# Kernel optimization log

Measured on AMD Instinct MI355X. Metric: run time of the kernel, lower is better.

The kernel has to match this reference:

```python
import jax, jax.numpy as jnp
import numpy as np

# ---- dimensions ----
N = 16384      # nodes
E = 131072     # edges (avg degree 8)
F = 128        # scalar channel width == s_dim
L = 9          # spherical-harmonic components (lmax=2)
R = 8          # radial basis size
DOUT = L * F   # post-product node width (1152)
K = 1024       # fixed number of master nodes (static stand-in for m>0.5)
HID = 64       # master-selection hidden dim
DA = 64        # virtual-attention head dim
LAMBDA_ATTN = 0.5
R_CUT = 5.0
EPS = 1e-9


def sh_l2(u):
    # real SH polynomials up to l=2 on unit vectors u[..., 3] -> [..., 9]
    x, y, z = u[..., 0], u[..., 1], u[..., 2]
    o = jnp.ones_like(x)
    return jnp.stack([o, x, y, z, x * y, y * z, 3.0 * z * z - 1.0, x * z, x * x - y * y], axis=-1)


def bessel(r):
    # Bessel radial basis; r [..., 1] -> [..., R]
    n = jnp.arange(1, R + 1, dtype=r.dtype)
    return jnp.sqrt(2.0 / R_CUT) * jnp.sin(n * jnp.pi * r / R_CUT) / jnp.maximum(r, EPS)


def setup_inputs() -> dict:
    key = jax.random.key(0)
    ks = jax.random.split(key, 18)
    s = lambda d: 1.0 / np.sqrt(d)
    return {
        'h': jax.random.normal(ks[0], (N, F), jnp.float32),
        'pos': 3.0 * jax.random.normal(ks[1], (N, 3), jnp.float32),
        'edge_sh': jax.random.normal(ks[2], (E, L), jnp.float32),
        'edge_feats': jax.random.uniform(ks[3], (E, R), jnp.float32),
        'W_node_l': s(F) * jax.random.normal(ks[4], (F, F), jnp.float32),
        'W_rad_l': s(R) * jax.random.normal(ks[5], (R, F), jnp.float32),
        'W_prod_l': s(L * F) * jax.random.normal(ks[6], (L, F, DOUT), jnp.float32),
        'ms_W1': s(F) * jax.random.normal(ks[7], (F, HID), jnp.float32),
        'ms_b1': jnp.zeros((HID,), jnp.float32),
        'ms_W2': s(HID) * jax.random.normal(ks[8], (HID, 1), jnp.float32),
        'ms_b2': jnp.zeros((1,), jnp.float32),
        'vg_Wq': s(F) * jax.random.normal(ks[9], (F, DA), jnp.float32),
        'vg_Wk': s(F) * jax.random.normal(ks[10], (F, DA), jnp.float32),
        'W_node_h': s(DOUT) * jax.random.normal(ks[11], (DOUT, F), jnp.float32),
        'W_rad_h': s(R) * jax.random.normal(ks[12], (R, F), jnp.float32),
        'W_prod_h': s(L * F) * jax.random.normal(ks[13], (L, F, DOUT), jnp.float32),
        'edge_index': jax.random.randint(ks[14], (2, E), 0, N),
    }


def reference(h, pos, edge_sh, edge_feats, W_node_l, W_rad_l, W_prod_l,
              ms_W1, ms_b1, ms_W2, ms_b2, vg_Wq, vg_Wk,
              W_node_h, W_rad_h, W_prod_h, edge_index):
    src, dst = edge_index[0], edge_index[1]

    # ---- local conv + reshape + prod (with padded residual sc) ----
    t = (h[src] @ W_node_l) * (edge_feats @ W_rad_l)                      # [E,F]
    msg = edge_sh[:, :, None] * t[:, None, :]                             # [E,L,F]
    upd = jax.ops.segment_sum(msg, dst, num_segments=N)                   # [N,L,F]
    sc = jnp.pad(h, ((0, 0), (0, DOUT - F)))
    h_local = jnp.einsum('nlf,lfg->ng', upd, W_prod_l) + sc               # [N,DOUT]

    # ---- master selection (MLP -> sigmoid); fixed top-K masters ----
    hs = h_local[:, :F]
    m = jax.nn.sigmoid(jax.nn.relu(hs @ ms_W1 + ms_b1) @ ms_W2 + ms_b2)[:, 0]  # [N]
    _, midx = jax.lax.top_k(m, K)
    master_idx = jnp.sort(midx)                                           # [K]

    # ---- induced subgraph among masters as dense [K,K] adjacency ----
    rank = jnp.full((N,), K, dtype=jnp.int32).at[master_idx].set(jnp.arange(K, dtype=jnp.int32))
    adj = jnp.zeros((K + 1, K + 1), h.dtype).at[rank[src], rank[dst]].max(jnp.ones((E,), h.dtype))
    adj_induced = adj[:K, :K]

    h_m = h_local[master_idx]                                             # [K,DOUT]
    pos_m = pos[master_idx]                                               # [K,3]
    hms = h_m[:, :F]

    # ---- virtual graph generation (attention -> thresholded dense adj) ----
    q = hms @ vg_Wq
    kk = hms @ vg_Wk
    A = jax.nn.sigmoid(q @ kk.T / jnp.sqrt(jnp.asarray(DA, h.dtype)))     # [K,K]
    A_virtual = jnp.where(A > LAMBDA_ATTN, A, 0.0)
    eye = jnp.eye(K, dtype=bool)
    Bv = (A_virtual > 0) & ~eye                                           # remove self loops
    Bv = Bv | Bv.T                                                        # to_undirected
    adj_master = jnp.clip(adj_induced + Bv.astype(h.dtype), 0.0, 1.0) * (1.0 - jnp.eye(K, dtype=h.dtype))

    # ---- hierarchical conv over dense master graph ----
    A_rec = adj_master.T                                                  # A_rec[i,j]=1: sender j -> receiver i
    V = pos_m[None, :, :] - pos_m[:, None, :]                             # vec = pos[src]-pos[dst]
    r = jnp.linalg.norm(V, axis=-1, keepdims=True)                        # [K,K,1]
    u = V / jnp.maximum(r, EPS)
    sh_m = sh_l2(u)                                                       # [K,K,L]
    rad = bessel(r)                                                       # [K,K,R]
    tm = (h_m @ W_node_h)[None, :, :] * (rad @ W_rad_h) * A_rec[:, :, None]  # [K,K,F]
    upd_m = jnp.einsum('ijl,ijf->ilf', sh_m, tm)                          # [K,L,F]
    h_hier = jnp.einsum('ilf,lfg->ig', upd_m, W_prod_h) + h_m             # sc_master pad is 0-width

    # ---- masked scatter blend ----
    h_exp = jnp.zeros_like(h_local).at[master_idx].set(h_hier)
    h_final = (1.0 - m[:, None]) * h_local + m[:, None] * h_exp
    return (h_final, A_virtual, m, master_idx)
```

## Files before the change

### kernel.cpp

```cpp
#include <hip/hip_runtime.h>
#include <hip/hip_bf16.h>
#include <stdint.h>

#define N_NODES 16384
#define E_EDGES 131072
#define F_DIM 128
#define L_DIM 9
#define R_DIM 8
#define DOUT_DIM 1152
#define K_SEL 1024
#define HID_DIM 64
#define DA_DIM 64

typedef unsigned short u16;
typedef __attribute__((ext_vector_type(8))) short bf16x8;
typedef __attribute__((ext_vector_type(4))) float f32x4;

static __device__ inline u16 f2bs(float x) {
  union { __hip_bfloat16 b; u16 s; } u;
  u.b = __float2bfloat16(x);
  return u.s;
}

#define GLDS16(gsrc, ldst) __builtin_amdgcn_global_load_lds( \
    (__attribute__((address_space(1))) void*)(void*)(gsrc),  \
    (__attribute__((address_space(3))) void*)(ldst), 16, 0, 0)

__global__ __launch_bounds__(256) void gemm_mfma(
    const float* __restrict__ A, const u16* __restrict__ Bt,
    float* __restrict__ C, int ldc, int M, int Nc, int Kc,
    const float* __restrict__ Add, int ldadd, int addW)
{
  __shared__ float Af[128 * 32];
  __shared__ u16  Bs[128 * 32];
  const int tid = threadIdx.x;
  const int wave = tid >> 6, lane = tid & 63;
  const int wm = wave >> 1, wn = wave & 1;
  const int l15 = lane & 15, quad = lane >> 4;
  const int bm = blockIdx.y * 128, bn = blockIdx.x * 128;

  f32x4 acc[4][4];
#pragma unroll
  for (int i = 0; i < 4; i++)
#pragma unroll
    for (int j = 0; j < 4; j++) acc[i][j] = (f32x4)(0.f);

  for (int k0 = 0; k0 < Kc; k0 += 32) {
    __syncthreads();
#pragma unroll
    for (int it = 0; it < 4; it++) {
      int c = it * 256 + tid;
      int row = c >> 3, op = c & 7;
      int oct = op ^ (row & 7);
      const float* g = A + (size_t)(bm + row) * Kc + k0 + oct * 4;
      GLDS16(g, &Af[c * 4]);
    }
#pragma unroll
    for (int it = 0; it < 2; it++) {
      int c = it * 256 + tid;
      int row = c >> 2, qp = c & 3;
      int q = qp ^ ((row >> 1) & 3);
      const u16* g = Bt + (size_t)(bn + row) * Kc + k0 + q * 8;
      GLDS16(g, &Bs[c * 8]);
    }
    __syncthreads();

    bf16x8 af[4], bfg[4];
#pragma unroll
    for (int mi = 0; mi < 4; mi++) {
      int m = wm * 64 + mi * 16 + l15;
      int o0 = (quad * 2) ^ (m & 7), o1 = (quad * 2 + 1) ^ (m & 7);
      float4 lo = *(const float4*)&Af[m * 32 + o0 * 4];
      float4 hi = *(const float4*)&Af[m * 32 + o1 * 4];
      bf16x8 r;
      r[0] = (short)f2bs(lo.x); r[1] = (short)f2bs(lo.y);
      r[2] = (short)f2bs(lo.z); r[3] = (short)f2bs(lo.w);
      r[4] = (short)f2bs(hi.x); r[5] = (short)f2bs(hi.y);
      r[6] = (short)f2bs(hi.z); r[7] = (short)f2bs(hi.w);
      af[mi] = r;
    }
#pragma unroll
    for (int ni = 0; ni < 4; ni++) {
      int n = wn * 64 + ni * 16 + l15;
      int q2 = quad ^ ((n >> 1) & 3);
      bfg[ni] = *(const bf16x8*)&Bs[n * 32 + q2 * 8];
    }
#pragma unroll
    for (int mi = 0; mi < 4; mi++)
#pragma unroll
      for (int ni = 0; ni < 4; ni++)
        acc[mi][ni] = __builtin_amdgcn_mfma_f32_16x16x32_bf16(af[mi], bfg[ni], acc[mi][ni], 0, 0, 0);
  }
#pragma unroll
  for (int mi = 0; mi < 4; mi++)
#pragma unroll
    for (int ni = 0; ni < 4; ni++)
#pragma unroll
      for (int r = 0; r < 4; r++) {
        int row = bm + wm * 64 + mi * 16 + quad * 4 + r;
        int col = bn + wn * 64 + ni * 16 + l15;
        float v = acc[mi][ni][r];
        if (Add != nullptr && col < addW) v += Add[(size_t)row * ldadd + col];
        C[(size_t)row * ldc + col] = v;
      }
}

__global__ __launch_bounds__(256) void gemm_mfma_b16(
    const u16* __restrict__ A, const u16* __restrict__ Bt,
    float* __restrict__ C, int ldc, int Kc, int nbx, int nwg,
    const float* __restrict__ Add, int ldadd, int addW)
{
  __shared__ u16 As[2][128 * 32];
  __shared__ u16 Bs[2][128 * 32];
  const int tid = threadIdx.x;
  const int wave = tid >> 6, lane = tid & 63;
  const int wm = wave >> 1, wn = wave & 1;
  const int l15 = lane & 15, quad = lane >> 4;
  const int lin = blockIdx.x;
  const int swz = (lin & 7) * (nwg >> 3) + (lin >> 3);
  const int bm = (swz / nbx) * 128, bn = (swz % nbx) * 128;

  const int c0 = tid,      r0 = c0 >> 2, q0 = (c0 & 3) ^ ((r0 >> 1) & 3);
  const int c1 = 256 + tid, r1 = c1 >> 2, q1 = (c1 & 3) ^ ((r1 >> 1) & 3);
  const u16* gA0 = A + (size_t)(bm + r0) * Kc + q0 * 8;
  const u16* gA1 = A + (size_t)(bm + r1) * Kc + q1 * 8;
  const u16* gB0 = Bt + (size_t)(bn + r0) * Kc + q0 * 8;
  const u16* gB1 = Bt + (size_t)(bn + r1) * Kc + q1 * 8;

  f32x4 acc[4][4];
#pragma unroll
  for (int i = 0; i < 4; i++)
#pragma unroll
    for (int j = 0; j < 4; j++) acc[i][j] = (f32x4)(0.f);

#define STAGE_AB(s, k0) do {                      \
    GLDS16(gA0 + (k0), &As[s][c0 * 8]);           \
    GLDS16(gA1 + (k0), &As[s][c1 * 8]);           \
    GLDS16(gB0 + (k0), &Bs[s][c0 * 8]);           \
    GLDS16(gB1 + (k0), &Bs[s][c1 * 8]);           \
  } while (0)

  STAGE_AB(0, 0);
  __syncthreads();
  int cur = 0;
  const int nt = Kc / 32;
  for (int t = 0; t < nt; t++) {
    if (t + 1 < nt) STAGE_AB(cur ^ 1, (t + 1) * 32);
    bf16x8 af[4], bfg[4];
#pragma unroll
    for (int mi = 0; mi < 4; mi++) {
      int m = wm * 64 + mi * 16 + l15;
      af[mi] = *(const bf16x8*)&As[cur][m * 32 + (quad ^ ((m >> 1) & 3)) * 8];
    }
#pragma unroll
    for (int ni = 0; ni < 4; ni++) {
      int n = wn * 64 + ni * 16 + l15;
      bfg[ni] = *(const bf16x8*)&Bs[cur][n * 32 + (quad ^ ((n >> 1) & 3)) * 8];
    }
#pragma unroll
    for (int mi = 0; mi < 4; mi++)
#pragma unroll
      for (int ni = 0; ni < 4; ni++)
        acc[mi][ni] = __builtin_amdgcn_mfma_f32_16x16x32_bf16(af[mi], bfg[ni], acc[mi][ni], 0, 0, 0);
    __syncthreads();
    cur ^= 1;
  }
#undef STAGE_AB

#pragma unroll
  for (int mi = 0; mi < 4; mi++)
#pragma unroll
    for (int ni = 0; ni < 4; ni++)
#pragma unroll
      for (int r = 0; r < 4; r++) {
        int row = bm + wm * 64 + mi * 16 + quad * 4 + r;
        int col = bn + wn * 64 + ni * 16 + l15;
        float v = acc[mi][ni][r];
        if (Add != nullptr && col < addW) v += Add[(size_t)row * ldadd + col];
        C[(size_t)row * ldc + col] = v;
      }
}

__global__ __launch_bounds__(256) void transpose_bf16(
    const float* __restrict__ W, u16* __restrict__ Bt, int K, int N)
{
  __shared__ float t[32][33];
  const int n0 = blockIdx.x * 32, k0 = blockIdx.y * 32;
  const int tx = threadIdx.x & 31, ty = threadIdx.x >> 5;
  for (int r = ty; r < 32; r += 8) t[r][tx] = W[(size_t)(k0 + r) * N + n0 + tx];
  __syncthreads();
  for (int r = ty; r < 32; r += 8) Bt[(size_t)(n0 + r) * K + k0 + tx] = f2bs(t[tx][r]);
}

__global__ __launch_bounds__(256) void hs_gemm_kernel(
    const float* __restrict__ A,
    const float* __restrict__ B,
    float* __restrict__ psum)
{
  __shared__ float As[16][129];
  __shared__ float Bs[16][128];
  const int tid = threadIdx.x;
  const int tx = tid & 15, ty = tid >> 4;
  const int bm = blockIdx.x * 128;
  const int z = blockIdx.y;
  const int kb = z * (DOUT_DIM / 4);
  const int ke = kb + DOUT_DIM / 4;
  const int ac = tid & 15, ar0 = tid >> 4;
  const int bc = tid & 127, br0 = tid >> 7;
  float acc[8][8];
#pragma unroll
  for (int i = 0; i < 8; i++)
#pragma unroll
    for (int j = 0; j < 8; j++) acc[i][j] = 0.f;

  float ra[8], rb[8];
#define LOADREG(k0) do {                                                       \
    _Pragma("unroll")                                                          \
    for (int rr = 0; rr < 8; rr++)                                             \
      ra[rr] = A[(size_t)(bm + ar0 + rr * 16) * DOUT_DIM + (k0) + ac];         \
    _Pragma("unroll")                                                          \
    for (int rr = 0; rr < 8; rr++)                                             \
      rb[rr] = B[(size_t)((k0) + br0 + rr * 2) * DOUT_DIM + bc];               \
  } while (0)

  LOADREG(kb);
  for (int k0 = kb; k0 < ke; k0 += 16) {
#pragma unroll
    for (int rr = 0; rr < 8; rr++) As[ac][ar0 + rr * 16] = ra[rr];
#pragma unroll
    for (int rr = 0; rr < 8; rr++) Bs[br0 + rr * 2][bc] = rb[rr];
    __syncthreads();
    if (k0 + 16 < ke) LOADREG(k0 + 16);
#pragma unroll
    for (int kk = 0; kk < 16; kk++) {
      float a[8], b[8];
#pragma unroll
      for (int i = 0; i < 8; i++) a[i] = As[kk][ty * 8 + i];
#pragma unroll
      for (int j = 0; j < 8; j++) b[j] = Bs[kk][tx * 8 + j];
#pragma unroll
      for (int i = 0; i < 8; i++)
#pragma unroll
        for (int j = 0; j < 8; j++) acc[i][j] = fmaf(a[i], b[j], acc[i][j]);
    }
    __syncthreads();
  }
#undef LOADREG
#pragma unroll
  for (int i = 0; i < 8; i++) {
    size_t row = (size_t)z * N_NODES + bm + ty * 8 + i;
#pragma unroll
    for (int j = 0; j < 8; j++)
      psum[row * F_DIM + tx * 8 + j] = acc[i][j];
  }
}

__global__ __launch_bounds__(256) void hs_reduce_kernel(
    const float* __restrict__ psum, const float* __restrict__ h, float* __restrict__ hs)
{
  size_t i4 = (size_t)blockIdx.x * 256 + threadIdx.x;
  const size_t stride = (size_t)N_NODES * F_DIM / 4;
  const float4* p = (const float4*)psum;
  float4 a = p[i4], b = p[i4 + stride], c = p[i4 + 2 * stride], d = p[i4 + 3 * stride];
  float4 hh = ((const float4*)h)[i4];
  float4 o;
  o.x = a.x + b.x + c.x + d.x + hh.x;
  o.y = a.y + b.y + c.y + d.y + hh.y;
  o.z = a.z + b.z + c.z + d.z + hh.z;
  o.w = a.w + b.w + c.w + d.w + hh.w;
  ((float4*)hs)[i4] = o;
}

__global__ __launch_bounds__(256) void gemm64_f32(
    const float* __restrict__ A, int lda,
    const float* __restrict__ B, int ldb,
    float* __restrict__ C, int ldc,
    int M, int Nc, int Kc, int kPerSplit,
    const float* __restrict__ Add, int ldadd, int addW)
{
  __shared__ float As[16][65];
  __shared__ float Bs[16][64];
  const int tid = threadIdx.x;
  const int tx = tid & 15, ty = tid >> 4;
  const int bm = blockIdx.y * 64, bn = blockIdx.x * 64;
  const int kb = blockIdx.z * kPerSplit;
  const int ke = min(kb + kPerSplit, Kc);
  float acc[4][4];
#pragma unroll
  for (int i = 0; i < 4; i++)
#pragma unroll
    for (int j = 0; j < 4; j++) acc[i][j] = 0.f;
  for (int k0 = kb; k0 < ke; k0 += 16) {
    const int ac = tid & 15, ar = tid >> 4;
#pragma unroll
    for (int rr = 0; rr < 4; rr++) {
      int row = ar + rr * 16;
      As[ac][row] = A[(size_t)(bm + row) * lda + k0 + ac];
    }
    const int bc = tid & 63, br = tid >> 6;
#pragma unroll
    for (int rr = 0; rr < 4; rr++) {
      int kr = br + rr * 4;
      Bs[kr][bc] = B[(size_t)(k0 + kr) * ldb + bn + bc];
    }
    __syncthreads();
#pragma unroll
    for (int kk = 0; kk < 16; kk++) {
      float a[4], b[4];
#pragma unroll
      for (int i = 0; i < 4; i++) a[i] = As[kk][ty * 4 + i];
#pragma unroll
      for (int j = 0; j < 4; j++) b[j] = Bs[kk][tx * 4 + j];
#pragma unroll
      for (int i = 0; i < 4; i++)
#pragma unroll
        for (int j = 0; j < 4; j++) acc[i][j] = fmaf(a[i], b[j], acc[i][j]);
    }
    __syncthreads();
  }
#pragma unroll
  for (int i = 0; i < 4; i++) {
    int row = bm + ty * 4 + i;
#pragma unroll
    for (int j = 0; j < 4; j++) {
      int col = bn + tx * 4 + j;
      if (gridDim.z > 1) {
        atomicAdd(&C[(size_t)row * ldc + col], acc[i][j]);
      } else {
        float v = acc[i][j];
        if (Add != nullptr && col < addW) v += Add[(size_t)row * ldadd + col];
        C[(size_t)row * ldc + col] = v;
      }
    }
  }
}

__global__ __launch_bounds__(256) void count_kernel(
    const int* __restrict__ ei, int* __restrict__ counts)
{
  int e = blockIdx.x * 256 + threadIdx.x;
  atomicAdd(&counts[ei[E_EDGES + e]], 1);
}

__global__ __launch_bounds__(1024) void scan_kernel(
    const int* __restrict__ counts, int* __restrict__ offsets, int* __restrict__ cursor)
{
  __shared__ int part[1024];
  const int t = threadIdx.x;
  const int base = t * 16;
  int loc[16];
  int s = 0;
#pragma unroll
  for (int k = 0; k < 16; k++) { loc[k] = counts[base + k]; s += loc[k]; }
  part[t] = s;
  __syncthreads();
  for (int d = 1; d < 1024; d <<= 1) {
    int v = (t >= d) ? part[t - d] : 0;
    __syncthreads();
    part[t] += v;
    __syncthreads();
  }
  int run = part[t] - s;
#pragma unroll
  for (int k = 0; k < 16; k++) {
    offsets[base + k] = run;
    cursor[base + k] = run;
    run += loc[k];
  }
}

__global__ __launch_bounds__(256) void fill_kernel(
    const int* __restrict__ ei, int* __restrict__ cursor, int* __restrict__ elist)
{
  int e = blockIdx.x * 256 + threadIdx.x;
  int d = ei[E_EDGES + e];
  int p = atomicAdd(&cursor[d], 1);
  elist[p] = e;
}

__global__ __launch_bounds__(128) void gather_accum_kernel(
    const float* __restrict__ hW, const float* __restrict__ edge_sh,
    const float* __restrict__ edge_feats, const float* __restrict__ W_rad_l,
    const int* __restrict__ ei, const int* __restrict__ offsets,
    const int* __restrict__ counts, const int* __restrict__ elist,
    float* __restrict__ upd, u16* __restrict__ updb)
{
  const int d = blockIdx.x, f = threadIdx.x;
  const float w0 = W_rad_l[0 * F_DIM + f], w1 = W_rad_l[1 * F_DIM + f];
  const float w2 = W_rad_l[2 * F_DIM + f], w3 = W_rad_l[3 * F_DIM + f];
  const float w4 = W_rad_l[4 * F_DIM + f], w5 = W_rad_l[5 * F_DIM + f];
  const float w6 = W_rad_l[6 * F_DIM + f], w7 = W_rad_l[7 * F_DIM + f];
  const int b = offsets[d], n = counts[d];
  float acc[L_DIM];
#pragma unroll
  for (int l = 0; l < L_DIM; l++) acc[l] = 0.f;
  for (int k = 0; k < n; k++) {
    const int e = elist[b + k];
    const int s = ei[e];
    const float4 ef0 = *(const float4*)&edge_feats[(size_t)e * R_DIM];
    const float4 ef1 = *(const float4*)&edge_feats[(size_t)e * R_DIM + 4];
    float rw = ef0.x * w0;
    rw = fmaf(ef0.y, w1, rw); rw = fmaf(ef0.z, w2, rw); rw = fmaf(ef0.w, w3, rw);
    rw = fmaf(ef1.x, w4, rw); rw = fmaf(ef1.y, w5, rw);
    rw = fmaf(ef1.z, w6, rw); rw = fmaf(ef1.w, w7, rw);
    const float tf = hW[(size_t)s * F_DIM + f] * rw;
#pragma unroll
    for (int l = 0; l < L_DIM; l++)
      acc[l] = fmaf(edge_sh[(size_t)e * L_DIM + l], tf, acc[l]);
  }
#pragma unroll
  for (int l = 0; l < L_DIM; l++)
    upd[(size_t)d * DOUT_DIM + l * F_DIM + f] = acc[l];
  if (updb != nullptr) {
#pragma unroll
    for (int l = 0; l < L_DIM; l++)
      updb[(size_t)d * DOUT_DIM + l * F_DIM + f] = f2bs(acc[l]);
  }
}

__global__ __launch_bounds__(256) void gate_kernel(
    const float* __restrict__ hs, const float* __restrict__ W1,
    const float* __restrict__ b1, const float* __restrict__ W2,
    const float* __restrict__ b2, float* __restrict__ m_ws, float* __restrict__ m_out,
    int* __restrict__ hist1)
{
  __shared__ float sW1[F_DIM * HID_DIM];
  __shared__ float srow[4][F_DIM];
  const int tid = threadIdx.x;
  for (int t = tid; t < F_DIM * HID_DIM; t += 256) sW1[t] = W1[t];
  const int wave = tid >> 6, lane = tid & 63;
  const int n = blockIdx.x * 4 + wave;
  srow[wave][lane] = hs[(size_t)n * F_DIM + lane];
  srow[wave][lane + 64] = hs[(size_t)n * F_DIM + lane + 64];
  __syncthreads();
  float hid = b1[lane];
#pragma unroll 8
  for (int c = 0; c < F_DIM; c++) hid = fmaf(srow[wave][c], sW1[c * HID_DIM + lane], hid);
  hid = fmaxf(hid, 0.f);
  float v = hid * W2[lane];
#pragma unroll
  for (int off = 32; off > 0; off >>= 1) v += __shfl_down(v, off);
  if (lane == 0) {
    float mm = 1.f / (1.f + expf(-(v + b2[0])));
    m_ws[n] = mm;
    m_out[n] = mm;
    unsigned mb = __float_as_uint(mm);
    atomicAdd(&hist1[mb >> 16], 1);
  }
}

__global__ __launch_bounds__(1024) void radix_sel_kernel(
    const int* __restrict__ hist, const int* __restrict__ kin, int kinIdx,
    int* __restrict__ outp, int outIdx)
{
  __shared__ int part[1024];
  const int t = threadIdx.x;
  const int Kv = kin ? kin[kinIdx] : K_SEL;
  const int base = t * 64;
  int s = 0;
  for (int k = 0; k < 64; k++) s += hist[base + k];
  part[t] = s;
  __syncthreads();
  for (int d = 1; d < 1024; d <<= 1) {
    int v = (t + d < 1024) ? part[t + d] : 0;
    __syncthreads();
    part[t] += v;
    __syncthreads();
  }
  int inc = part[t];
  if (inc >= Kv && inc - s < Kv) {
    int r = inc - s;
    for (int b = base + 63; b >= base; b--) {
      int hv = hist[b];
      if (r + hv >= Kv) { outp[outIdx] = b; outp[outIdx + 1] = Kv - r; break; }
      r += hv;
    }
  }
}

__global__ __launch_bounds__(256) void hist2_kernel(
    const float* __restrict__ m_ws, const int* __restrict__ selb, int* __restrict__ hist2)
{
  int i = blockIdx.x * 256 + threadIdx.x;
  unsigned mb = __float_as_uint(m_ws[i]);
  if ((int)(mb >> 16) == selb[0]) atomicAdd(&hist2[mb & 0xFFFFu], 1);
}

__global__ __launch_bounds__(256) void flag_kernel(
    const float* __restrict__ m_ws, int* __restrict__ selb,
    unsigned char* __restrict__ flags, int* __restrict__ cand)
{
  int i = blockIdx.x * 256 + threadIdx.x;
  unsigned mb = __float_as_uint(m_ws[i]);
  unsigned vb = ((unsigned)selb[0] << 16) | (unsigned)selb[2];
  unsigned char fl = 0;
  if (mb > vb) fl = 1;
  else if (mb == vb) { int p = atomicAdd(&selb[4], 1); cand[p] = i; }
  flags[i] = fl;
}

__global__ __launch_bounds__(1024) void cand_kernel(
    const int* __restrict__ selb, const int* __restrict__ cand, unsigned char* __restrict__ flags)
{
  const int nc = selb[4], need = selb[3];
  for (int c = threadIdx.x; c < nc; c += 1024) {
    const int idx = cand[c];
    int r = 0;
    for (int o = 0; o < nc; o++) r += (cand[o] < idx) ? 1 : 0;
    if (r < need) flags[idx] = 1;
  }
}

__global__ __launch_bounds__(1024) void compact_kernel(
    const unsigned char* __restrict__ flags, int* __restrict__ midx,
    int* __restrict__ rank, float* __restrict__ mi_out)
{
  __shared__ int part[1024];
  const int t = threadIdx.x;
  const int base = t * 16;
  int loc[16];
  int s = 0;
#pragma unroll
  for (int k = 0; k < 16; k++) { loc[k] = flags[base + k]; s += loc[k]; }
  part[t] = s;
  __syncthreads();
  for (int d = 1; d < 1024; d <<= 1) {
    int v = (t >= d) ? part[t - d] : 0;
    __syncthreads();
    part[t] += v;
    __syncthreads();
  }
  int run = part[t] - s;
#pragma unroll
  for (int k = 0; k < 16; k++) {
    int i = base + k;
    if (loc[k]) {
      midx[run] = i;
      mi_out[run] = (float)i;
      rank[i] = run;
      run++;
    } else {
      rank[i] = K_SEL;
    }
  }
}

__global__ __launch_bounds__(256) void adj_kernel(
    const int* __restrict__ ei, const int* __restrict__ rank, unsigned char* __restrict__ adjm)
{
  int e = blockIdx.x * 256 + threadIdx.x;
  int rs = rank[ei[e]];
  int rd = rank[ei[E_EDGES + e]];
  if (rs < K_SEL && rd < K_SEL) adjm[(size_t)rs * K_SEL + rd] = 1;
}

__global__ __launch_bounds__(128) void gather_kernel(
    const float* __restrict__ hl, const float* __restrict__ pos,
    const int* __restrict__ midx, float* __restrict__ h_m, float* __restrict__ pos_m)
{
  const int rI = blockIdx.x, t = threadIdx.x;
  const int mi = midx[rI];
  const float4* src = (const float4*)(hl + (size_t)mi * DOUT_DIM);
  float4* dst = (float4*)(h_m + (size_t)rI * DOUT_DIM);
  for (int c = t; c < DOUT_DIM / 4; c += 128) dst[c] = src[c];
  if (t < 3) pos_m[rI * 3 + t] = pos[mi * 3 + t];
}

__global__ __launch_bounds__(128) void qk_kernel(
    const float* __restrict__ hs, const int* __restrict__ midx,
    const float* __restrict__ Wq, const float* __restrict__ Wk,
    float* __restrict__ q, float* __restrict__ kk)
{
  __shared__ float row[F_DIM];
  const int i = blockIdx.x, t = threadIdx.x;
  const int mi = midx[i];
  row[t] = hs[(size_t)mi * F_DIM + t];
  __syncthreads();
  const int d = t & 63;
  const float* W = (t < 64) ? Wq : Wk;
  float acc = 0.f;
#pragma unroll 8
  for (int c = 0; c < F_DIM; c++) acc = fmaf(row[c], W[c * DA_DIM + d], acc);
  float* dst = (t < 64) ? q : kk;
  dst[(size_t)i * DA_DIM + d] = acc;
}

__global__ __launch_bounds__(256) void attn_kernel(
    const float* __restrict__ q, const float* __restrict__ kk,
    unsigned char* __restrict__ maskA, float* __restrict__ Av)
{
  __shared__ float qs[16][DA_DIM + 1], ks[16][DA_DIM + 1];
  const int tx = threadIdx.x, ty = threadIdx.y;
  const int tid = ty * 16 + tx;
  const int i0 = blockIdx.y * 16, j0 = blockIdx.x * 16;
  for (int t = tid; t < 16 * DA_DIM; t += 256) {
    int rr = t >> 6, cc = t & 63;
    qs[rr][cc] = q[(size_t)(i0 + rr) * DA_DIM + cc];
    ks[rr][cc] = kk[(size_t)(j0 + rr) * DA_DIM + cc];
  }
  __syncthreads();
  float acc = 0.f;
#pragma unroll
  for (int d2 = 0; d2 < DA_DIM; d2++) acc = fmaf(qs[ty][d2], ks[tx][d2], acc);
  float sgl = 1.f / (1.f + expf(-acc * 0.125f));
  size_t o = (size_t)(i0 + ty) * K_SEL + (j0 + tx);
  bool big = sgl > 0.5f;
  maskA[o] = big ? 1 : 0;
  Av[o] = big ? sgl : 0.f;
}

__global__ __launch_bounds__(256) void listbuild_kernel(
    const unsigned char* __restrict__ adjm, const unsigned char* __restrict__ maskA,
    u16* __restrict__ list, int* __restrict__ nj)
{
  __shared__ int cnt;
  const int i = blockIdx.x, tid = threadIdx.x;
  const int lane = tid & 63;
  if (tid == 0) cnt = 0;
  __syncthreads();
#pragma unroll
  for (int jt = 0; jt < 4; jt++) {
    int j = jt * 256 + tid;
    bool e = (j != i) && (adjm[(size_t)j * K_SEL + i] | maskA[(size_t)j * K_SEL + i] |
                          maskA[(size_t)i * K_SEL + j]);
    unsigned long long m = __ballot(e);
    int nset = __popcll(m);
    int base = 0;
    if (lane == 0 && nset) base = atomicAdd(&cnt, nset);
    base = __shfl(base, 0);
    if (e) {
      int p = base + __popcll(m & ((1ull << lane) - 1ull));
      list[(size_t)i * K_SEL + p] = (u16)j;
    }
  }
  __syncthreads();
  if (tid == 0) nj[i] = cnt;
}

__global__ __launch_bounds__(512) void hier2_kernel(
    const float* __restrict__ hWn, const float* __restrict__ pos_m,
    const float* __restrict__ W_rad_h, const u16* __restrict__ list,
    const int* __restrict__ nj, float* __restrict__ upd_m, u16* __restrict__ updb_m)
{
  __shared__ float gsm[128][20];
  __shared__ float red[3][L_DIM][F_DIM];
  const int tid = threadIdx.x;
  const int i = blockIdx.x;
  const int f = tid & 127, jsub = tid >> 7;
  const float sw0 = W_rad_h[0 * F_DIM + f], sw1 = W_rad_h[1 * F_DIM + f];
  const float sw2 = W_rad_h[2 * F_DIM + f], sw3 = W_rad_h[3 * F_DIM + f];
  const float sw4 = W_rad_h[4 * F_DIM + f], sw5 = W_rad_h[5 * F_DIM + f];
  const float sw6 = W_rad_h[6 * F_DIM + f], sw7 = W_rad_h[7 * F_DIM + f];
  const float pix = pos_m[i * 3 + 0], piy = pos_m[i * 3 + 1], piz = pos_m[i * 3 + 2];
  float acc[L_DIM];
#pragma unroll
  for (int l = 0; l < L_DIM; l++) acc[l] = 0.f;
  const int n = nj[i];
  for (int c0 = 0; c0 < n; c0 += 128) {
    const int cnt = min(128, n - c0);
    __syncthreads();
    if (tid < cnt) {
      const int j = list[(size_t)i * K_SEL + c0 + tid];
      float vx = pos_m[j * 3 + 0] - pix;
      float vy = pos_m[j * 3 + 1] - piy;
      float vz = pos_m[j * 3 + 2] - piz;
      float r = sqrtf(vx * vx + vy * vy + vz * vz);
      float rm = fmaxf(r, 1e-9f);
      float inv = 1.f / rm;
      float ux = vx * inv, uy = vy * inv, uz = vz * inv;
      float theta = 0.62831853071795864769f * r;
      float s1 = sinf(theta), c1 = cosf(theta);
      float coef = 0.632455532033675866f * inv;
      float snm2 = 0.f, snm1 = s1;
      gsm[tid][0] = s1 * coef;
#pragma unroll
      for (int nn = 2; nn <= R_DIM; nn++) {
        float sn = 2.f * c1 * snm1 - snm2;
        gsm[tid][nn - 1] = sn * coef;
        snm2 = snm1; snm1 = sn;
      }
      gsm[tid][8] = 1.f; gsm[tid][9] = ux; gsm[tid][10] = uy; gsm[tid][11] = uz;
      gsm[tid][12] = ux * uy; gsm[tid][13] = uy * uz;
      gsm[tid][14] = 3.f * uz * uz - 1.f;
      gsm[tid][15] = ux * uz; gsm[tid][16] = ux * ux - uy * uy;
      gsm[tid][17] = __int_as_float(j);
      gsm[tid][18] = 0.f; gsm[tid][19] = 0.f;
    }
    __syncthreads();
    for (int t = jsub; t < cnt; t += 4) {
      float2 s2 = *(const float2*)&gsm[t][16];
      const int j = __float_as_int(s2.y);
      const float hw = hWn[(size_t)j * F_DIM + f];
      float4 r0 = *(const float4*)&gsm[t][0];
      float4 r1 = *(const float4*)&gsm[t][4];
      float4 s0 = *(const float4*)&gsm[t][8];
      float4 s1g = *(const float4*)&gsm[t][12];
      float rw = r0.x * sw0;
      rw = fmaf(r0.y, sw1, rw); rw = fmaf(r0.z, sw2, rw); rw = fmaf(r0.w, sw3, rw);
      rw = fmaf(r1.x, sw4, rw); rw = fmaf(r1.y, sw5, rw);
      rw = fmaf(r1.z, sw6, rw); rw = fmaf(r1.w, sw7, rw);
      const float tm = hw * rw;
      acc[0] = fmaf(s0.x, tm, acc[0]); acc[1] = fmaf(s0.y, tm, acc[1]);
      acc[2] = fmaf(s0.z, tm, acc[2]); acc[3] = fmaf(s0.w, tm, acc[3]);
      acc[4] = fmaf(s1g.x, tm, acc[4]); acc[5] = fmaf(s1g.y, tm, acc[5]);
      acc[6] = fmaf(s1g.z, tm, acc[6]); acc[7] = fmaf(s1g.w, tm, acc[7]);
      acc[8] = fmaf(s2.x, tm, acc[8]);
    }
  }
  __syncthreads();
  if (jsub > 0) {
#pragma unroll
    for (int l = 0; l < L_DIM; l++) red[jsub - 1][l][f] = acc[l];
  }
  __syncthreads();
  if (jsub == 0) {
#pragma unroll
    for (int l = 0; l < L_DIM; l++) {
      float v = acc[l] + red[0][l][f] + red[1][l][f] + red[2][l][f];
      upd_m[(size_t)i * DOUT_DIM + l * F_DIM + f] = v;
      updb_m[(size_t)i * DOUT_DIM + l * F_DIM + f] = f2bs(v);
    }
  }
}

__global__ __launch_bounds__(256) void combine_kernel(
    float* __restrict__ out0, const float* __restrict__ h_hier,
    const float* __restrict__ m_ws, const int* __restrict__ rank)
{
  size_t i4 = (size_t)blockIdx.x * 256 + threadIdx.x;
  int n = (int)(i4 / (DOUT_DIM / 4));
  int g4 = (int)(i4 % (DOUT_DIM / 4));
  float mv = m_ws[n];
  int r = rank[n];
  float4 hl = ((const float4*)out0)[i4];
  float4 he = make_float4(0.f, 0.f, 0.f, 0.f);
  if (r < K_SEL) he = ((const float4*)h_hier)[(size_t)r * (DOUT_DIM / 4) + g4];
  float4 o;
  o.x = (1.f - mv) * hl.x + mv * he.x;
  o.y = (1.f - mv) * hl.y + mv * he.y;
  o.z = (1.f - mv) * hl.z + mv * he.z;
  o.w = (1.f - mv) * hl.w + mv * he.w;
  ((float4*)out0)[i4] = o;
}

extern "C" void kernel_launch(void* const* d_in, const int* in_sizes, int n_in,
                              void* d_out, int out_size, void* d_ws, size_t ws_size,
                              hipStream_t stream)
{
  const float* h         = (const float*)d_in[0];
  const float* pos       = (const float*)d_in[1];
  const float* edge_sh   = (const float*)d_in[2];
  const float* edge_feats= (const float*)d_in[3];
  const float* W_node_l  = (const float*)d_in[4];
  const float* W_rad_l   = (const float*)d_in[5];
  const float* W_prod_l  = (const float*)d_in[6];
  const float* ms_W1     = (const float*)d_in[7];
  const float* ms_b1     = (const float*)d_in[8];
  const float* ms_W2     = (const float*)d_in[9];
  const float* ms_b2     = (const float*)d_in[10];
  const float* vg_Wq     = (const float*)d_in[11];
  const float* vg_Wk     = (const float*)d_in[12];
  const float* W_node_h  = (const float*)d_in[13];
  const float* W_rad_h   = (const float*)d_in[14];
  const float* W_prod_h  = (const float*)d_in[15];
  const int*   eidx      = (const int*)d_in[16];

  float* out    = (float*)d_out;
  float* out_hf = out;
  float* out_Av = out + (size_t)N_NODES * DOUT_DIM;
  float* out_m  = out_Av + (size_t)K_SEL * K_SEL;
  float* out_mi = out_m + N_NODES;

  char* ws = (char*)d_ws;
  float* upd = (float*)ws;
  float* hW  = (float*)(ws + (size_t)N_NODES * DOUT_DIM * 4);
  float* hs  = hW;
  const size_t updbOff = (size_t)N_NODES * DOUT_DIM * 4 + (size_t)N_NODES * F_DIM * 4;
  const size_t updbNeed = updbOff + (size_t)N_NODES * DOUT_DIM * 2;
  const bool useB16 = (ws_size >= updbNeed);
  u16* updb = (u16*)(ws + updbOff);
  float* psum = out_hf;
  u16* Btl = (u16*)out_Av;
  char* csr = (char*)out_Av + (((size_t)DOUT_DIM * DOUT_DIM * 2 + 255) & ~(size_t)255);
  int* counts  = (int*)csr;
  int* offsets = counts + N_NODES;
  int* cursor  = offsets + N_NODES;
  int* elist   = cursor + N_NODES;
  size_t off = 0;
  auto alloc = [&](size_t bytes) -> void* {
    void* p = ws + off;
    off += (bytes + 255) & ~(size_t)255;
    return p;
  };
  float* m_ws  = (float*)alloc((size_t)N_NODES * 4);
  int*   rank  = (int*)alloc((size_t)N_NODES * 4);
  int*   midx  = (int*)alloc((size_t)K_SEL * 4);
  int*   hist1 = (int*)alloc((size_t)65536 * 4);
  int*   hist2 = (int*)alloc((size_t)65536 * 4);
  int*   selb  = (int*)alloc((size_t)64 * 4);
  int*   cand  = (int*)alloc((size_t)N_NODES * 4);
  unsigned char* flags = (unsigned char*)alloc((size_t)N_NODES);
  unsigned char* adjm  = (unsigned char*)alloc((size_t)K_SEL * K_SEL);
  unsigned char* maskA = (unsigned char*)alloc((size_t)K_SEL * K_SEL);
  float* qbuf  = (float*)alloc((size_t)K_SEL * DA_DIM * 4);
  float* kbuf  = (float*)alloc((size_t)K_SEL * DA_DIM * 4);
  float* h_m   = (float*)alloc((size_t)K_SEL * DOUT_DIM * 4);
  float* pos_m = (float*)alloc((size_t)K_SEL * 3 * 4);
  float* hWn   = (float*)alloc((size_t)K_SEL * F_DIM * 4);
  float* upd_m = (float*)alloc((size_t)K_SEL * DOUT_DIM * 4);
  float* h_hier= (float*)alloc((size_t)K_SEL * DOUT_DIM * 4);
  u16*   Bth   = (u16*)alloc((size_t)DOUT_DIM * DOUT_DIM * 2);
  u16*   jlist = (u16*)alloc((size_t)K_SEL * K_SEL * 2);
  int*   njbuf = (int*)alloc((size_t)K_SEL * 4);
  u16*   updbm = (u16*)alloc((size_t)K_SEL * DOUT_DIM * 2);

  hipMemsetAsync(counts, 0, (size_t)N_NODES * 4, stream);
  transpose_bf16<<<dim3(DOUT_DIM / 32, DOUT_DIM / 32), 256, 0, stream>>>(
      W_prod_l, Btl, DOUT_DIM, DOUT_DIM);
  gemm64_f32<<<dim3(F_DIM / 64, N_NODES / 64, 1), 256, 0, stream>>>(
      h, F_DIM, W_node_l, F_DIM, hW, F_DIM, N_NODES, F_DIM, F_DIM, F_DIM, nullptr, 0, 0);
  count_kernel<<<E_EDGES / 256, 256, 0, stream>>>(eidx, counts);
  scan_kernel<<<1, 1024, 0, stream>>>(counts, offsets, cursor);
  fill_kernel<<<E_EDGES / 256, 256, 0, stream>>>(eidx, cursor, elist);
  gather_accum_kernel<<<N_NODES, 128, 0, stream>>>(
      hW, edge_sh, edge_feats, W_rad_l, eidx, offsets, counts, elist, upd,
      useB16 ? updb : nullptr);
  hs_gemm_kernel<<<dim3(N_NODES / 128, 4), 256, 0, stream>>>(upd, W_prod_l, psum);
  hs_reduce_kernel<<<(N_NODES * F_DIM / 4) / 256, 256, 0, stream>>>(psum, h, hs);
  if (useB16) {
    gemm_mfma_b16<<<(DOUT_DIM / 128) * (N_NODES / 128), 256, 0, stream>>>(
        updb, Btl, out_hf, DOUT_DIM, DOUT_DIM, DOUT_DIM / 128,
        (DOUT_DIM / 128) * (N_NODES / 128), h, F_DIM, F_DIM);
  } else {
    gemm_mfma<<<dim3(DOUT_DIM / 128, N_NODES / 128), 256, 0, stream>>>(
        upd, Btl, out_hf, DOUT_DIM, N_NODES, DOUT_DIM, DOUT_DIM, h, F_DIM, F_DIM);
  }

  hipMemsetAsync(adjm, 0, (size_t)K_SEL * K_SEL, stream);
  hipMemsetAsync(hist1, 0, (size_t)65536 * 4 * 2 + 256, stream);
  transpose_bf16<<<dim3(DOUT_DIM / 32, DOUT_DIM / 32), 256, 0, stream>>>(
      W_prod_h, Bth, DOUT_DIM, DOUT_DIM);
  gate_kernel<<<N_NODES / 4, 256, 0, stream>>>(hs, ms_W1, ms_b1, ms_W2, ms_b2,
                                               m_ws, out_m, hist1);
  radix_sel_kernel<<<1, 1024, 0, stream>>>(hist1, nullptr, 0, selb, 0);
  hist2_kernel<<<N_NODES / 256, 256, 0, stream>>>(m_ws, selb, hist2);
  radix_sel_kernel<<<1, 1024, 0, stream>>>(hist2, selb, 1, selb, 2);
  flag_kernel<<<N_NODES / 256, 256, 0, stream>>>(m_ws, selb, flags, cand);
  cand_kernel<<<1, 1024, 0, stream>>>(selb, cand, flags);
  compact_kernel<<<1, 1024, 0, stream>>>(flags, midx, rank, out_mi);
  adj_kernel<<<E_EDGES / 256, 256, 0, stream>>>(eidx, rank, adjm);
  gather_kernel<<<K_SEL, 128, 0, stream>>>(out_hf, pos, midx, h_m, pos_m);
  qk_kernel<<<K_SEL, 128, 0, stream>>>(hs, midx, vg_Wq, vg_Wk, qbuf, kbuf);
  attn_kernel<<<dim3(K_SEL / 16, K_SEL / 16), dim3(16, 16), 0, stream>>>(qbuf, kbuf, maskA, out_Av);
  listbuild_kernel<<<K_SEL, 256, 0, stream>>>(adjm, maskA, jlist, njbuf);
  hipMemsetAsync(hWn, 0, (size_t)K_SEL * F_DIM * 4, stream);
  gemm64_f32<<<dim3(F_DIM / 64, K_SEL / 64, 4), 256, 0, stream>>>(
      h_m, DOUT_DIM, W_node_h, F_DIM, hWn, F_DIM,
      K_SEL, F_DIM, DOUT_DIM, DOUT_DIM / 4, nullptr, 0, 0);
  hier2_kernel<<<K_SEL, 512, 0, stream>>>(hWn, pos_m, W_rad_h, jlist, njbuf, upd_m, updbm);
  gemm_mfma_b16<<<(DOUT_DIM / 128) * (K_SEL / 128), 256, 0, stream>>>(
      updbm, Bth, h_hier, DOUT_DIM, DOUT_DIM, DOUT_DIM / 128,
      (DOUT_DIM / 128) * (K_SEL / 128), h_m, DOUT_DIM, DOUT_DIM);
  combine_kernel<<<(N_NODES * DOUT_DIM / 4) / 256, 256, 0, stream>>>(out_hf, h_hier, m_ws, rank);
}
```

Before: 664.3 us.

## Build transposed adjacency/mask for coalesced list build; split hier2 across two blocks

The adjacency and attention-mask kernels now also write transposed copies. This lets the neighbour-list builder read one contiguous row per block with vector loads instead of strided column reads. The hierarchical accumulation kernel now uses two 256-thread blocks per master node, each taking alternate 128-neighbour chunks with a 2-way unrolled inner loop. The two partial sums are written to a buffer and combined and converted to bf16 by a new finalize kernel. In exchange, the attention kernel does extra scattered byte writes, the code assumes adjT sits directly after adjm in memory so a single memset clears both, and there is one extra launch plus more global traffic for the partial sums.

```diff
diff --git a/kernel.cpp b/kernel.cpp
--- a/kernel.cpp
+++ b/kernel.cpp
@@ -546,12 +546,16 @@
 }
 
 __global__ __launch_bounds__(256) void adj_kernel(
-    const int* __restrict__ ei, const int* __restrict__ rank, unsigned char* __restrict__ adjm)
+    const int* __restrict__ ei, const int* __restrict__ rank,
+    unsigned char* __restrict__ adjm, unsigned char* __restrict__ adjT)
 {
   int e = blockIdx.x * 256 + threadIdx.x;
   int rs = rank[ei[e]];
   int rd = rank[ei[E_EDGES + e]];
-  if (rs < K_SEL && rd < K_SEL) adjm[(size_t)rs * K_SEL + rd] = 1;
+  if (rs < K_SEL && rd < K_SEL) {
+    adjm[(size_t)rs * K_SEL + rd] = 1;
+    adjT[(size_t)rd * K_SEL + rs] = 1;
+  }
 }
 
 __global__ __launch_bounds__(128) void gather_kernel(
@@ -587,7 +591,8 @@
 
 __global__ __launch_bounds__(256) void attn_kernel(
     const float* __restrict__ q, const float* __restrict__ kk,
-    unsigned char* __restrict__ maskA, float* __restrict__ Av)
+    unsigned char* __restrict__ maskA, unsigned char* __restrict__ maskAT,
+    float* __restrict__ Av)
 {
   __shared__ float qs[16][DA_DIM + 1], ks[16][DA_DIM + 1];
   const int tx = threadIdx.x, ty = threadIdx.y;
@@ -605,24 +610,32 @@
   float sgl = 1.f / (1.f + expf(-acc * 0.125f));
   size_t o = (size_t)(i0 + ty) * K_SEL + (j0 + tx);
   bool big = sgl > 0.5f;
-  maskA[o] = big ? 1 : 0;
+  unsigned char bb = big ? 1 : 0;
+  maskA[o] = bb;
+  maskAT[(size_t)(j0 + tx) * K_SEL + (i0 + ty)] = bb;
   Av[o] = big ? sgl : 0.f;
 }
 
 __global__ __launch_bounds__(256) void listbuild_kernel(
-    const unsigned char* __restrict__ adjm, const unsigned char* __restrict__ maskA,
-    u16* __restrict__ list, int* __restrict__ nj)
+    const unsigned char* __restrict__ adjT, const unsigned char* __restrict__ maskAT,
+    const unsigned char* __restrict__ maskA, u16* __restrict__ list, int* __restrict__ nj)
 {
   __shared__ int cnt;
   const int i = blockIdx.x, tid = threadIdx.x;
   const int lane = tid & 63;
   if (tid == 0) cnt = 0;
   __syncthreads();
-#pragma unroll
-  for (int jt = 0; jt < 4; jt++) {
-    int j = jt * 256 + tid;
-    bool e = (j != i) && (adjm[(size_t)j * K_SEL + i] | maskA[(size_t)j * K_SEL + i] |
-                          maskA[(size_t)i * K_SEL + j]);
+  const int j0 = tid * 4;
+  uchar4 a  = *(const uchar4*)&adjT  [(size_t)i * K_SEL + j0];
+  uchar4 mt = *(const uchar4*)&maskAT[(size_t)i * K_SEL + j0];
+  uchar4 ma = *(const uchar4*)&maskA [(size_t)i * K_SEL + j0];
+  unsigned char av[4];
+  av[0] = a.x | mt.x | ma.x; av[1] = a.y | mt.y | ma.y;
+  av[2] = a.z | mt.z | ma.z; av[3] = a.w | mt.w | ma.w;
+#pragma unroll
+  for (int r = 0; r < 4; r++) {
+    int j = j0 + r;
+    bool e = (j != i) && av[r];
     unsigned long long m = __ballot(e);
     int nset = __popcll(m);
     int base = 0;
@@ -637,26 +650,48 @@
   if (tid == 0) nj[i] = cnt;
 }
 
-__global__ __launch_bounds__(512) void hier2_kernel(
+__global__ __launch_bounds__(256) void hier2_kernel(
     const float* __restrict__ hWn, const float* __restrict__ pos_m,
     const float* __restrict__ W_rad_h, const u16* __restrict__ list,
-    const int* __restrict__ nj, float* __restrict__ upd_m, u16* __restrict__ updb_m)
+    const int* __restrict__ nj, float* __restrict__ psum2)
 {
   __shared__ float gsm[128][20];
-  __shared__ float red[3][L_DIM][F_DIM];
+  __shared__ float red[L_DIM][F_DIM];
   const int tid = threadIdx.x;
-  const int i = blockIdx.x;
+  const int i = blockIdx.x >> 1, half = blockIdx.x & 1;
   const int f = tid & 127, jsub = tid >> 7;
   const float sw0 = W_rad_h[0 * F_DIM + f], sw1 = W_rad_h[1 * F_DIM + f];
   const float sw2 = W_rad_h[2 * F_DIM + f], sw3 = W_rad_h[3 * F_DIM + f];
   const float sw4 = W_rad_h[4 * F_DIM + f], sw5 = W_rad_h[5 * F_DIM + f];
   const float sw6 = W_rad_h[6 * F_DIM + f], sw7 = W_rad_h[7 * F_DIM + f];
+  const float* hWf = hWn + f;
   const float pix = pos_m[i * 3 + 0], piy = pos_m[i * 3 + 1], piz = pos_m[i * 3 + 2];
   float acc[L_DIM];
 #pragma unroll
   for (int l = 0; l < L_DIM; l++) acc[l] = 0.f;
   const int n = nj[i];
-  for (int c0 = 0; c0 < n; c0 += 128) {
+
+#define HBODY(tt)                                                        \
+  { float2 s2 = *(const float2*)&gsm[tt][16];                            \
+    const int jj = __float_as_int(s2.y);                                 \
+    const float hw = hWf[(size_t)jj * F_DIM];                            \
+    float4 r0 = *(const float4*)&gsm[tt][0];                             \
+    float4 r1 = *(const float4*)&gsm[tt][4];                             \
+    float4 s0 = *(const float4*)&gsm[tt][8];                             \
+    float4 s1g = *(const float4*)&gsm[tt][12];                           \
+    float rw = r0.x * sw0;                                               \
+    rw = fmaf(r0.y, sw1, rw); rw = fmaf(r0.z, sw2, rw);                  \
+    rw = fmaf(r0.w, sw3, rw); rw = fmaf(r1.x, sw4, rw);                  \
+    rw = fmaf(r1.y, sw5, rw); rw = fmaf(r1.z, sw6, rw);                  \
+    rw = fmaf(r1.w, sw7, rw);                                            \
+    const float tm = hw * rw;                                            \
+    acc[0] = fmaf(s0.x, tm, acc[0]); acc[1] = fmaf(s0.y, tm, acc[1]);    \
+    acc[2] = fmaf(s0.z, tm, acc[2]); acc[3] = fmaf(s0.w, tm, acc[3]);    \
+    acc[4] = fmaf(s1g.x, tm, acc[4]); acc[5] = fmaf(s1g.y, tm, acc[5]);  \
+    acc[6] = fmaf(s1g.z, tm, acc[6]); acc[7] = fmaf(s1g.w, tm, acc[7]);  \
+    acc[8] = fmaf(s2.x, tm, acc[8]); }
+
+  for (int c0 = half * 128; c0 < n; c0 += 256) {
     const int cnt = min(128, n - c0);
     __syncthreads();
     if (tid < cnt) {
@@ -684,43 +719,31 @@
       gsm[tid][14] = 3.f * uz * uz - 1.f;
       gsm[tid][15] = ux * uz; gsm[tid][16] = ux * ux - uy * uy;
       gsm[tid][17] = __int_as_float(j);
-      gsm[tid][18] = 0.f; gsm[tid][19] = 0.f;
-    }
-    __syncthreads();
-    for (int t = jsub; t < cnt; t += 4) {
-      float2 s2 = *(const float2*)&gsm[t][16];
-      const int j = __float_as_int(s2.y);
-      const float hw = hWn[(size_t)j * F_DIM + f];
-      float4 r0 = *(const float4*)&gsm[t][0];
-      float4 r1 = *(const float4*)&gsm[t][4];
-      float4 s0 = *(const float4*)&gsm[t][8];
-      float4 s1g = *(const float4*)&gsm[t][12];
-      float rw = r0.x * sw0;
-      rw = fmaf(r0.y, sw1, rw); rw = fmaf(r0.z, sw2, rw); rw = fmaf(r0.w, sw3, rw);
-      rw = fmaf(r1.x, sw4, rw); rw = fmaf(r1.y, sw5, rw);
-      rw = fmaf(r1.z, sw6, rw); rw = fmaf(r1.w, sw7, rw);
-      const float tm = hw * rw;
-      acc[0] = fmaf(s0.x, tm, acc[0]); acc[1] = fmaf(s0.y, tm, acc[1]);
-      acc[2] = fmaf(s0.z, tm, acc[2]); acc[3] = fmaf(s0.w, tm, acc[3]);
-      acc[4] = fmaf(s1g.x, tm, acc[4]); acc[5] = fmaf(s1g.y, tm, acc[5]);
-      acc[6] = fmaf(s1g.z, tm, acc[6]); acc[7] = fmaf(s1g.w, tm, acc[7]);
-      acc[8] = fmaf(s2.x, tm, acc[8]);
-    }
-  }
-  __syncthreads();
-  if (jsub > 0) {
-#pragma unroll
-    for (int l = 0; l < L_DIM; l++) red[jsub - 1][l][f] = acc[l];
+    }
+    __syncthreads();
+    int t = jsub;
+    for (; t + 2 < cnt; t += 4) { HBODY(t); HBODY(t + 2); }
+    for (; t < cnt; t += 2) { HBODY(t); }
+  }
+#undef HBODY
+  __syncthreads();
+  if (jsub == 1) {
+#pragma unroll
+    for (int l = 0; l < L_DIM; l++) red[l][f] = acc[l];
   }
   __syncthreads();
   if (jsub == 0) {
 #pragma unroll
-    for (int l = 0; l < L_DIM; l++) {
-      float v = acc[l] + red[0][l][f] + red[1][l][f] + red[2][l][f];
-      upd_m[(size_t)i * DOUT_DIM + l * F_DIM + f] = v;
-      updb_m[(size_t)i * DOUT_DIM + l * F_DIM + f] = f2bs(v);
-    }
-  }
+    for (int l = 0; l < L_DIM; l++)
+      psum2[((size_t)half * K_SEL + i) * DOUT_DIM + l * F_DIM + f] = acc[l] + red[l][f];
+  }
+}
+
+__global__ __launch_bounds__(256) void hier_fin_kernel(
+    const float* __restrict__ psum2, u16* __restrict__ updbm)
+{
+  size_t idx = (size_t)blockIdx.x * 256 + threadIdx.x;
+  updbm[idx] = f2bs(psum2[idx] + psum2[idx + (size_t)K_SEL * DOUT_DIM]);
 }
 
 __global__ __launch_bounds__(256) void combine_kernel(
@@ -801,13 +824,15 @@
   int*   cand  = (int*)alloc((size_t)N_NODES * 4);
   unsigned char* flags = (unsigned char*)alloc((size_t)N_NODES);
   unsigned char* adjm  = (unsigned char*)alloc((size_t)K_SEL * K_SEL);
+  unsigned char* adjT  = (unsigned char*)alloc((size_t)K_SEL * K_SEL);
   unsigned char* maskA = (unsigned char*)alloc((size_t)K_SEL * K_SEL);
+  unsigned char* maskAT= (unsigned char*)alloc((size_t)K_SEL * K_SEL);
   float* qbuf  = (float*)alloc((size_t)K_SEL * DA_DIM * 4);
   float* kbuf  = (float*)alloc((size_t)K_SEL * DA_DIM * 4);
   float* h_m   = (float*)alloc((size_t)K_SEL * DOUT_DIM * 4);
   float* pos_m = (float*)alloc((size_t)K_SEL * 3 * 4);
   float* hWn   = (float*)alloc((size_t)K_SEL * F_DIM * 4);
-  float* upd_m = (float*)alloc((size_t)K_SEL * DOUT_DIM * 4);
+  float* psum2 = (float*)alloc((size_t)2 * K_SEL * DOUT_DIM * 4);
   float* h_hier= (float*)alloc((size_t)K_SEL * DOUT_DIM * 4);
   u16*   Bth   = (u16*)alloc((size_t)DOUT_DIM * DOUT_DIM * 2);
   u16*   jlist = (u16*)alloc((size_t)K_SEL * K_SEL * 2);
@@ -836,7 +861,7 @@
         upd, Btl, out_hf, DOUT_DIM, N_NODES, DOUT_DIM, DOUT_DIM, h, F_DIM, F_DIM);
   }
 
-  hipMemsetAsync(adjm, 0, (size_t)K_SEL * K_SEL, stream);
+  hipMemsetAsync(adjm, 0, (size_t)2 * K_SEL * K_SEL, stream);
   hipMemsetAsync(hist1, 0, (size_t)65536 * 4 * 2 + 256, stream);
   transpose_bf16<<<dim3(DOUT_DIM / 32, DOUT_DIM / 32), 256, 0, stream>>>(
       W_prod_h, Bth, DOUT_DIM, DOUT_DIM);
@@ -848,16 +873,18 @@
   flag_kernel<<<N_NODES / 256, 256, 0, stream>>>(m_ws, selb, flags, cand);
   cand_kernel<<<1, 1024, 0, stream>>>(selb, cand, flags);
   compact_kernel<<<1, 1024, 0, stream>>>(flags, midx, rank, out_mi);
-  adj_kernel<<<E_EDGES / 256, 256, 0, stream>>>(eidx, rank, adjm);
+  adj_kernel<<<E_EDGES / 256, 256, 0, stream>>>(eidx, rank, adjm, adjT);
   gather_kernel<<<K_SEL, 128, 0, stream>>>(out_hf, pos, midx, h_m, pos_m);
   qk_kernel<<<K_SEL, 128, 0, stream>>>(hs, midx, vg_Wq, vg_Wk, qbuf, kbuf);
-  attn_kernel<<<dim3(K_SEL / 16, K_SEL / 16), dim3(16, 16), 0, stream>>>(qbuf, kbuf, maskA, out_Av);
-  listbuild_kernel<<<K_SEL, 256, 0, stream>>>(adjm, maskA, jlist, njbuf);
+  attn_kernel<<<dim3(K_SEL / 16, K_SEL / 16), dim3(16, 16), 0, stream>>>(
+      qbuf, kbuf, maskA, maskAT, out_Av);
+  listbuild_kernel<<<K_SEL, 256, 0, stream>>>(adjT, maskAT, maskA, jlist, njbuf);
   hipMemsetAsync(hWn, 0, (size_t)K_SEL * F_DIM * 4, stream);
   gemm64_f32<<<dim3(F_DIM / 64, K_SEL / 64, 4), 256, 0, stream>>>(
       h_m, DOUT_DIM, W_node_h, F_DIM, hWn, F_DIM,
       K_SEL, F_DIM, DOUT_DIM, DOUT_DIM / 4, nullptr, 0, 0);
-  hier2_kernel<<<K_SEL, 512, 0, stream>>>(hWn, pos_m, W_rad_h, jlist, njbuf, upd_m, updbm);
+  hier2_kernel<<<K_SEL * 2, 256, 0, stream>>>(hWn, pos_m, W_rad_h, jlist, njbuf, psum2);
+  hier_fin_kernel<<<(K_SEL * DOUT_DIM) / 256, 256, 0, stream>>>(psum2, updbm);
   gemm_mfma_b16<<<(DOUT_DIM / 128) * (K_SEL / 128), 256, 0, stream>>>(
       updbm, Bth, h_hier, DOUT_DIM, DOUT_DIM, DOUT_DIM / 128,
       (DOUT_DIM / 128) * (K_SEL / 128), h_m, DOUT_DIM, DOUT_DIM);
```

Measured after the change: 678.1 us. 2.1% more time.

## Use raw barriers with vmcnt waits in MFMA GEMM and transposed masks for listbuild

Applied to the files above, without the earlier changes.

The bf16 MFMA GEMM main loop replaces __syncthreads with s_barrier plus explicit s_waitcnt vmcnt. This lets the prefetch of the next LDS stage stay in flight while the current stage is consumed. Separately, adj_kernel and attn_kernel now also write transposed byte masks. listbuild can then read contiguous uchar4 rows instead of column-strided bytes. This costs extra strided byte writes and an additional 2MB of workspace.

```diff
diff --git a/kernel.cpp b/kernel.cpp
--- a/kernel.cpp
+++ b/kernel.cpp
@@ -139,13 +139,22 @@
     GLDS16(gB0 + (k0), &Bs[s][c0 * 8]);           \
     GLDS16(gB1 + (k0), &Bs[s][c1 * 8]);           \
   } while (0)
+#define RAWBAR() do { __builtin_amdgcn_s_barrier(); \
+    __builtin_amdgcn_sched_barrier(0); } while (0)
 
   STAGE_AB(0, 0);
-  __syncthreads();
+  asm volatile("s_waitcnt vmcnt(0)" ::: "memory");
+  RAWBAR();
   int cur = 0;
   const int nt = Kc / 32;
   for (int t = 0; t < nt; t++) {
-    if (t + 1 < nt) STAGE_AB(cur ^ 1, (t + 1) * 32);
+    if (t + 1 < nt) {
+      STAGE_AB(cur ^ 1, (t + 1) * 32);
+      asm volatile("s_waitcnt vmcnt(4)" ::: "memory");
+    } else {
+      asm volatile("s_waitcnt vmcnt(0)" ::: "memory");
+    }
+    RAWBAR();
     bf16x8 af[4], bfg[4];
 #pragma unroll
     for (int mi = 0; mi < 4; mi++) {
@@ -162,10 +171,11 @@
 #pragma unroll
       for (int ni = 0; ni < 4; ni++)
         acc[mi][ni] = __builtin_amdgcn_mfma_f32_16x16x32_bf16(af[mi], bfg[ni], acc[mi][ni], 0, 0, 0);
-    __syncthreads();
+    RAWBAR();
     cur ^= 1;
   }
 #undef STAGE_AB
+#undef RAWBAR
 
 #pragma unroll
   for (int mi = 0; mi < 4; mi++)
@@ -546,12 +556,16 @@
 }
 
 __global__ __launch_bounds__(256) void adj_kernel(
-    const int* __restrict__ ei, const int* __restrict__ rank, unsigned char* __restrict__ adjm)
+    const int* __restrict__ ei, const int* __restrict__ rank,
+    unsigned char* __restrict__ adjm, unsigned char* __restrict__ adjT)
 {
   int e = blockIdx.x * 256 + threadIdx.x;
   int rs = rank[ei[e]];
   int rd = rank[ei[E_EDGES + e]];
-  if (rs < K_SEL && rd < K_SEL) adjm[(size_t)rs * K_SEL + rd] = 1;
+  if (rs < K_SEL && rd < K_SEL) {
+    adjm[(size_t)rs * K_SEL + rd] = 1;
+    adjT[(size_t)rd * K_SEL + rs] = 1;
+  }
 }
 
 __global__ __launch_bounds__(128) void gather_kernel(
@@ -587,7 +601,8 @@
 
 __global__ __launch_bounds__(256) void attn_kernel(
     const float* __restrict__ q, const float* __restrict__ kk,
-    unsigned char* __restrict__ maskA, float* __restrict__ Av)
+    unsigned char* __restrict__ maskA, unsigned char* __restrict__ maskAT,
+    float* __restrict__ Av)
 {
   __shared__ float qs[16][DA_DIM + 1], ks[16][DA_DIM + 1];
   const int tx = threadIdx.x, ty = threadIdx.y;
@@ -605,24 +620,32 @@
   float sgl = 1.f / (1.f + expf(-acc * 0.125f));
   size_t o = (size_t)(i0 + ty) * K_SEL + (j0 + tx);
   bool big = sgl > 0.5f;
-  maskA[o] = big ? 1 : 0;
+  unsigned char bb = big ? 1 : 0;
+  maskA[o] = bb;
+  maskAT[(size_t)(j0 + tx) * K_SEL + (i0 + ty)] = bb;
   Av[o] = big ? sgl : 0.f;
 }
 
 __global__ __launch_bounds__(256) void listbuild_kernel(
-    const unsigned char* __restrict__ adjm, const unsigned char* __restrict__ maskA,
-    u16* __restrict__ list, int* __restrict__ nj)
+    const unsigned char* __restrict__ adjT, const unsigned char* __restrict__ maskAT,
+    const unsigned char* __restrict__ maskA, u16* __restrict__ list, int* __restrict__ nj)
 {
   __shared__ int cnt;
   const int i = blockIdx.x, tid = threadIdx.x;
   const int lane = tid & 63;
   if (tid == 0) cnt = 0;
   __syncthreads();
-#pragma unroll
-  for (int jt = 0; jt < 4; jt++) {
-    int j = jt * 256 + tid;
-    bool e = (j != i) && (adjm[(size_t)j * K_SEL + i] | maskA[(size_t)j * K_SEL + i] |
-                          maskA[(size_t)i * K_SEL + j]);
+  const int j0 = tid * 4;
+  uchar4 a  = *(const uchar4*)&adjT  [(size_t)i * K_SEL + j0];
+  uchar4 mt = *(const uchar4*)&maskAT[(size_t)i * K_SEL + j0];
+  uchar4 ma = *(const uchar4*)&maskA [(size_t)i * K_SEL + j0];
+  unsigned char av[4];
+  av[0] = a.x | mt.x | ma.x; av[1] = a.y | mt.y | ma.y;
+  av[2] = a.z | mt.z | ma.z; av[3] = a.w | mt.w | ma.w;
+#pragma unroll
+  for (int r = 0; r < 4; r++) {
+    int j = j0 + r;
+    bool e = (j != i) && av[r];
     unsigned long long m = __ballot(e);
     int nset = __popcll(m);
     int base = 0;
@@ -801,7 +824,9 @@
   int*   cand  = (int*)alloc((size_t)N_NODES * 4);
   unsigned char* flags = (unsigned char*)alloc((size_t)N_NODES);
   unsigned char* adjm  = (unsigned char*)alloc((size_t)K_SEL * K_SEL);
+  unsigned char* adjT  = (unsigned char*)alloc((size_t)K_SEL * K_SEL);
   unsigned char* maskA = (unsigned char*)alloc((size_t)K_SEL * K_SEL);
+  unsigned char* maskAT= (unsigned char*)alloc((size_t)K_SEL * K_SEL);
   float* qbuf  = (float*)alloc((size_t)K_SEL * DA_DIM * 4);
   float* kbuf  = (float*)alloc((size_t)K_SEL * DA_DIM * 4);
   float* h_m   = (float*)alloc((size_t)K_SEL * DOUT_DIM * 4);
@@ -836,7 +861,7 @@
         upd, Btl, out_hf, DOUT_DIM, N_NODES, DOUT_DIM, DOUT_DIM, h, F_DIM, F_DIM);
   }
 
-  hipMemsetAsync(adjm, 0, (size_t)K_SEL * K_SEL, stream);
+  hipMemsetAsync(adjm, 0, (size_t)2 * K_SEL * K_SEL, stream);
   hipMemsetAsync(hist1, 0, (size_t)65536 * 4 * 2 + 256, stream);
   transpose_bf16<<<dim3(DOUT_DIM / 32, DOUT_DIM / 32), 256, 0, stream>>>(
       W_prod_h, Bth, DOUT_DIM, DOUT_DIM);
@@ -848,11 +873,12 @@
   flag_kernel<<<N_NODES / 256, 256, 0, stream>>>(m_ws, selb, flags, cand);
   cand_kernel<<<1, 1024, 0, stream>>>(selb, cand, flags);
   compact_kernel<<<1, 1024, 0, stream>>>(flags, midx, rank, out_mi);
-  adj_kernel<<<E_EDGES / 256, 256, 0, stream>>>(eidx, rank, adjm);
+  adj_kernel<<<E_EDGES / 256, 256, 0, stream>>>(eidx, rank, adjm, adjT);
   gather_kernel<<<K_SEL, 128, 0, stream>>>(out_hf, pos, midx, h_m, pos_m);
   qk_kernel<<<K_SEL, 128, 0, stream>>>(hs, midx, vg_Wq, vg_Wk, qbuf, kbuf);
-  attn_kernel<<<dim3(K_SEL / 16, K_SEL / 16), dim3(16, 16), 0, stream>>>(qbuf, kbuf, maskA, out_Av);
-  listbuild_kernel<<<K_SEL, 256, 0, stream>>>(adjm, maskA, jlist, njbuf);
+  attn_kernel<<<dim3(K_SEL / 16, K_SEL / 16), dim3(16, 16), 0, stream>>>(
+      qbuf, kbuf, maskA, maskAT, out_Av);
+  listbuild_kernel<<<K_SEL, 256, 0, stream>>>(adjT, maskAT, maskA, jlist, njbuf);
   hipMemsetAsync(hWn, 0, (size_t)K_SEL * F_DIM * 4, stream);
   gemm64_f32<<<dim3(F_DIM / 64, K_SEL / 64, 4), 256, 0, stream>>>(
       h_m, DOUT_DIM, W_node_h, F_DIM, hWn, F_DIM,
```

Result: no change. 667.8 us (+0.5%).
